# Kernel tuning notes

Measured on AMD Instinct MI355X. Metric: run time of the kernel, lower is better.

The kernel has to match this reference:

```python
import math
import jax, jax.numpy as jnp
import numpy as np

INPUT_DIM = 512
HIDDEN_DIM = 512
BATCH = 8
SEQ_LEN = 4096


def _xavier(key, shape):
    fan_out, fan_in = shape
    limit = math.sqrt(6.0 / (fan_in + fan_out))
    return jax.random.uniform(key, shape, jnp.float32, -limit, limit)


def setup_inputs() -> dict:
    key = jax.random.key(0)
    kx, kA, kB, kC, kD, kWg = jax.random.split(key, 6)
    return {
        "x": jax.random.normal(kx, (BATCH, SEQ_LEN, INPUT_DIM), jnp.float32),
        "A": jax.random.uniform(kA, (HIDDEN_DIM,), jnp.float32, 0.8, 0.95),
        "B": _xavier(kB, (HIDDEN_DIM, INPUT_DIM)),
        "C": _xavier(kC, (HIDDEN_DIM, HIDDEN_DIM)),
        "D": _xavier(kD, (HIDDEN_DIM, INPUT_DIM)),
        "Wg": _xavier(kWg, (HIDDEN_DIM, INPUT_DIM)),
        "bias_h": jnp.zeros((HIDDEN_DIM,), jnp.float32),
        "bias_y": jnp.zeros((HIDDEN_DIM,), jnp.float32),
    }


def reference(x, A, B, C, D, Wg, bias_h, bias_y):
    # x: (b, t, i). Eval mode: dropout is identity.
    hidden_dim = A.shape[0]
    # Precompute all input-dependent per-step terms as batched GEMMs.
    g = jnp.clip(jax.nn.sigmoid(jnp.einsum('bti,hi->bth', x, Wg)), 0.05, 0.95)
    xB = jnp.einsum('bti,hi->bth', x, B)
    # h_t = h_{t-1} + g_t*(A*h_{t-1} + xB_t + bias_h - h_{t-1})
    #     = (1 - g_t*(1 - A)) * h_{t-1} + g_t*(xB_t + bias_h)
    a_coef = 1.0 - g * (1.0 - A)          # (b, t, h)
    b_coef = g * (xB + bias_h)            # (b, t, h)

    def step(h, ab):
        a_t, b_t = ab
        h = a_t * h + b_t
        return h, h

    h0 = jnp.zeros((x.shape[0], hidden_dim), x.dtype)
    _, hs = jax.lax.scan(step, h0, (jnp.swapaxes(a_coef, 0, 1), jnp.swapaxes(b_coef, 0, 1)))
    hs = jnp.swapaxes(hs, 0, 1)           # (b, t, h)

    scale = 1.0 / math.sqrt(hidden_dim)
    y = (jnp.einsum('bth,oh->bto', hs, C) + jnp.einsum('bti,hi->bth', x, D) + bias_y) * scale
    return y
```

## Files before the change

kernel.cpp:

```cpp
#include <hip/hip_runtime.h>
#include <math.h>

#define MTOT 32768
#define KD 512
#define HD 512
#define NB 8
#define TS 4096
#define NCHUNK 64
#define TCHUNK 64

typedef __attribute__((ext_vector_type(8))) short bf16x8;
typedef __attribute__((ext_vector_type(4))) float f32x4;
typedef __attribute__((ext_vector_type(4))) unsigned short us4;

#define GLD16(gsrc, ldst) __builtin_amdgcn_global_load_lds( \
    (const __attribute__((address_space(1))) void*)(gsrc),   \
    (__attribute__((address_space(3))) void*)(ldst), 16, 0, 0)

__device__ __forceinline__ unsigned short f2bf(float f) {
    unsigned u = __float_as_uint(f);
    return (unsigned short)((u + 0x7FFFu + ((u >> 16) & 1u)) >> 16);
}
__device__ __forceinline__ float bf2f(unsigned short u) {
    return __uint_as_float(((unsigned)u) << 16);
}

__global__ __launch_bounds__(256) void cast_all(
    const float* __restrict__ x, const float* __restrict__ B,
    const float* __restrict__ G, const float* __restrict__ C,
    const float* __restrict__ D,
    unsigned short* __restrict__ x16, unsigned short* __restrict__ w16)
{
    const int blk = blockIdx.x;
    const float* src;
    unsigned short* dst;
    int i;
    if (blk < (MTOT * KD / 1024)) {
        src = x; dst = x16;
        i = blk * 1024 + threadIdx.x * 4;
    } else {
        const int r = blk - (MTOT * KD / 1024);
        const int mat = r >> 8;
        src = (mat == 0) ? B : (mat == 1) ? G : (mat == 2) ? C : D;
        dst = w16 + (size_t)mat * (HD * KD);
        i = (r & 255) * 1024 + threadIdx.x * 4;
    }
    float4 v = *(const float4*)(src + i);
    us4 o; o.x = f2bf(v.x); o.y = f2bf(v.y); o.z = f2bf(v.z); o.w = f2bf(v.w);
    *(us4*)(dst + i) = o;
}

__global__ __launch_bounds__(256, 2) void in_gemm_mfma(
    const short* __restrict__ xb, const short* __restrict__ wmat,
    const float* __restrict__ Avec, const float* __restrict__ bias_h,
    unsigned* __restrict__ ab16, float2* __restrict__ chPS)
{
    __shared__ __align__(16) short Xs[2][128 * 64];
    __shared__ __align__(16) short Ws[2][2][64 * 64];
    const int tid = threadIdx.x;
    const int w = tid >> 6, l = tid & 63;
    const int bid = blockIdx.x;
    const int xcd = bid & 7;
    const int jj  = bid >> 3;
    const int n0  = (jj & 7) * 64;
    const int m0  = (xcd * 32 + (jj >> 3)) * 128;
    const int wm = (w & 1) * 64;
    const int wn = (w >> 1) * 32;

    int xsrc[4], xdst[4];
    #pragma unroll
    for (int j = 0; j < 4; ++j) {
        const int s = (w * 4 + j) * 64 + l;
        const int r = s >> 3, g = (s & 7) ^ (r & 7);
        xsrc[j] = (m0 + r) * KD + g * 8;
        xdst[j] = (w * 4 + j) * 64 * 8;
    }
    int wsrc[2], wdst[2];
    #pragma unroll
    for (int j = 0; j < 2; ++j) {
        const int s = (w * 2 + j) * 64 + l;
        const int r = s >> 3, g = (s & 7) ^ (r & 7);
        wsrc[j] = (n0 + r) * KD + g * 8;
        wdst[j] = (w * 2 + j) * 64 * 8;
    }

#define STAGE_IN(TI, BUF) do {                                              \
    const int kk_ = (TI) * 64;                                              \
    _Pragma("unroll")                                                       \
    for (int j_ = 0; j_ < 4; ++j_)                                          \
        GLD16(xb + xsrc[j_] + kk_, &Xs[BUF][xdst[j_]]);                     \
    _Pragma("unroll")                                                       \
    for (int m_ = 0; m_ < 2; ++m_)                                          \
        _Pragma("unroll")                                                   \
        for (int j_ = 0; j_ < 2; ++j_)                                      \
            GLD16(wmat + (size_t)m_ * (HD * KD) + wsrc[j_] + kk_,           \
                  &Ws[BUF][m_][wdst[j_]]);                                  \
} while (0)

    f32x4 acc[2][4][2];
    #pragma unroll
    for (int a = 0; a < 2; ++a)
        #pragma unroll
        for (int i = 0; i < 4; ++i)
            #pragma unroll
            for (int j = 0; j < 2; ++j) acc[a][i][j] = (f32x4)0.0f;

    STAGE_IN(0, 0);
    STAGE_IN(1, 1);

    #pragma unroll
    for (int it = 0; it < 8; ++it) {
        const int cur = it & 1;
        if (it < 7) asm volatile("s_waitcnt vmcnt(8)" ::: "memory");
        else        asm volatile("s_waitcnt vmcnt(0)" ::: "memory");
        __builtin_amdgcn_s_barrier();
        __builtin_amdgcn_s_setprio(1);
        #pragma unroll
        for (int kc = 0; kc < 2; ++kc) {
            const int g = kc * 4 + (l >> 4);
            bf16x8 af[4];
            #pragma unroll
            for (int mt = 0; mt < 4; ++mt) {
                const int r = wm + mt * 16 + (l & 15);
                af[mt] = *(const bf16x8*)(&Xs[cur][r * 64 + ((g ^ (r & 7)) * 8)]);
            }
            #pragma unroll
            for (int mat = 0; mat < 2; ++mat) {
                #pragma unroll
                for (int nt = 0; nt < 2; ++nt) {
                    const int r = wn + nt * 16 + (l & 15);
                    bf16x8 bfv = *(const bf16x8*)(&Ws[cur][mat][r * 64 + ((g ^ (r & 7)) * 8)]);
                    #pragma unroll
                    for (int mt = 0; mt < 4; ++mt)
                        acc[mat][mt][nt] = __builtin_amdgcn_mfma_f32_16x16x32_bf16(
                            af[mt], bfv, acc[mat][mt][nt], 0, 0, 0);
                }
            }
        }
        __builtin_amdgcn_s_setprio(0);
        asm volatile("s_waitcnt lgkmcnt(0)" ::: "memory");
        __builtin_amdgcn_s_barrier();
        if (it < 6) STAGE_IN(it + 2, cur);
    }
#undef STAGE_IN

    const int q  = l >> 4;
    const int cl = l & 15;
    const int bidx   = m0 >> 12;
    const int c_in_b = ((m0 & (TS - 1)) >> 6) + (w & 1);
    #pragma unroll
    for (int nt = 0; nt < 2; ++nt) {
        const int n = n0 + wn + nt * 16 + cl;
        const float An1 = 1.0f - Avec[n];
        const float bh  = bias_h[n];
        float Pc = 1.0f, Sc = 0.0f;
        #pragma unroll
        for (int mt = 0; mt < 4; ++mt) {
            float Pl = 1.0f, Sl = 0.0f;
            #pragma unroll
            for (int r = 0; r < 4; ++r) {
                const float vB = acc[0][mt][nt][r];
                const float vG = acc[1][mt][nt][r];
                float g = __builtin_amdgcn_rcpf(1.0f + __expf(-vG));
                g = fminf(fmaxf(g, 0.05f), 0.95f);
                const unsigned short su = f2bf(g * An1);
                const unsigned short bu = f2bf(g * (vB + bh));
                const float a  = 1.0f - bf2f(su);
                const float bb = bf2f(bu);
                const int m = m0 + wm + mt * 16 + q * 4 + r;
                ab16[(size_t)m * HD + n] = (unsigned)su | ((unsigned)bu << 16);
                Sl = fmaf(a, Sl, bb);
                Pl *= a;
            }
            float Pm = 1.0f, Sm = 0.0f;
            #pragma unroll
            for (int k = 0; k < 4; ++k) {
                const float Pk = __shfl(Pl, cl + 16 * k, 64);
                const float Sk = __shfl(Sl, cl + 16 * k, 64);
                Sm = fmaf(Pk, Sm, Sk);
                Pm *= Pk;
            }
            Sc = fmaf(Pm, Sc, Sm);
            Pc *= Pm;
        }
        if (q == 0) {
            chPS[(size_t)c_in_b * (NB * HD) + bidx * HD + n] = make_float2(Pc, Sc);
        }
    }
}

__global__ __launch_bounds__(256) void scan_pass3(
    const unsigned* __restrict__ ab, const float2* __restrict__ chPS,
    unsigned short* __restrict__ hs_out)
{
    const int g = blockIdx.x * blockDim.x + threadIdx.x;
    const int h4 = (g & 127) * 4;
    const int rest = g >> 7;
    const int b = rest & (NB - 1);
    const int c = rest >> 3;
    const float2* p = chPS + (size_t)b * HD + h4;
    float hv0 = 0.0f, hv1 = 0.0f, hv2 = 0.0f, hv3 = 0.0f;
    for (int jc = 0; jc < c; ++jc) {
        const float4 ps01 = *(const float4*)(p + (size_t)jc * (NB * HD));
        const float4 ps23 = *(const float4*)(p + (size_t)jc * (NB * HD) + 2);
        hv0 = fmaf(ps01.x, hv0, ps01.y);
        hv1 = fmaf(ps01.z, hv1, ps01.w);
        hv2 = fmaf(ps23.x, hv2, ps23.y);
        hv3 = fmaf(ps23.z, hv3, ps23.w);
    }
    size_t idx = ((size_t)(b * TS + c * TCHUNK)) * HD + h4;
    #pragma unroll 4
    for (int t = 0; t < TCHUNK; ++t) {
        const uint4 v = *(const uint4*)(ab + idx);
        const float a0 = 1.0f - bf2f((unsigned short)(v.x & 0xFFFFu));
        const float a1 = 1.0f - bf2f((unsigned short)(v.y & 0xFFFFu));
        const float a2 = 1.0f - bf2f((unsigned short)(v.z & 0xFFFFu));
        const float a3 = 1.0f - bf2f((unsigned short)(v.w & 0xFFFFu));
        hv0 = fmaf(a0, hv0, bf2f((unsigned short)(v.x >> 16)));
        hv1 = fmaf(a1, hv1, bf2f((unsigned short)(v.y >> 16)));
        hv2 = fmaf(a2, hv2, bf2f((unsigned short)(v.z >> 16)));
        hv3 = fmaf(a3, hv3, bf2f((unsigned short)(v.w >> 16)));
        us4 o; o.x = f2bf(hv0); o.y = f2bf(hv1); o.z = f2bf(hv2); o.w = f2bf(hv3);
        *(us4*)(hs_out + idx) = o;
        idx += HD;
    }
}

__global__ __launch_bounds__(256, 2) void out_gemm_dual(
    const short* __restrict__ hs, const short* __restrict__ xb,
    const short* __restrict__ Cb, const short* __restrict__ Db,
    const float* __restrict__ bias_y, float* __restrict__ y)
{
    __shared__ __align__(16) short As[2][128 * 64];
    __shared__ __align__(16) short Ws[2][128 * 64];
    const int tid = threadIdx.x;
    const int w = tid >> 6, l = tid & 63;
    const int bid = blockIdx.x;
    const int xcd = bid & 7;
    const int jj  = bid >> 3;
    const int n0  = (jj & 3) * 128;
    const int m0  = (xcd * 32 + (jj >> 2)) * 128;
    const int wm = (w & 1) * 64;
    const int wn = (w >> 1) * 64;

    int aoff[4], woff[4], dst_s[4];
    #pragma unroll
    for (int j = 0; j < 4; ++j) {
        const int s = (w * 4 + j) * 64 + l;
        const int r = s >> 3, g = (s & 7) ^ (r & 7);
        aoff[j] = (m0 + r) * HD + g * 8;
        woff[j] = (n0 + r) * HD + g * 8;
        dst_s[j] = (w * 4 + j) * 64 * 8;
    }

#define STAGE_OUT(TI, BUF) do {                                         \
    const short* abase_ = (((TI) < 8) ? hs : xb) + ((TI) & 7) * 64;     \
    const short* wbase_ = (((TI) < 8) ? Cb : Db) + ((TI) & 7) * 64;     \
    _Pragma("unroll")                                                   \
    for (int j_ = 0; j_ < 4; ++j_) {                                    \
        GLD16(abase_ + aoff[j_], &As[BUF][dst_s[j_]]);                  \
        GLD16(wbase_ + woff[j_], &Ws[BUF][dst_s[j_]]);                  \
    }                                                                   \
} while (0)

    f32x4 acc[4][4];
    #pragma unroll
    for (int i = 0; i < 4; ++i)
        #pragma unroll
        for (int j = 0; j < 4; ++j) acc[i][j] = (f32x4)0.0f;

    STAGE_OUT(0, 0);
    STAGE_OUT(1, 1);

    #pragma unroll
    for (int ti = 0; ti < 16; ++ti) {
        const int cur = ti & 1;
        if (ti < 15) asm volatile("s_waitcnt vmcnt(8)" ::: "memory");
        else         asm volatile("s_waitcnt vmcnt(0)" ::: "memory");
        __builtin_amdgcn_s_barrier();
        __builtin_amdgcn_s_setprio(1);
        #pragma unroll
        for (int kc = 0; kc < 2; ++kc) {
            const int g = kc * 4 + (l >> 4);
            bf16x8 af[4], bfv[4];
            #pragma unroll
            for (int t = 0; t < 4; ++t) {
                const int ra = wm + t * 16 + (l & 15);
                af[t] = *(const bf16x8*)(&As[cur][ra * 64 + ((g ^ (ra & 7)) * 8)]);
                const int rb = wn + t * 16 + (l & 15);
                bfv[t] = *(const bf16x8*)(&Ws[cur][rb * 64 + ((g ^ (rb & 7)) * 8)]);
            }
            #pragma unroll
            for (int mt = 0; mt < 4; ++mt)
                #pragma unroll
                for (int nt = 0; nt < 4; ++nt)
                    acc[mt][nt] = __builtin_amdgcn_mfma_f32_16x16x32_bf16(
                        af[mt], bfv[nt], acc[mt][nt], 0, 0, 0);
        }
        __builtin_amdgcn_s_setprio(0);
        asm volatile("s_waitcnt lgkmcnt(0)" ::: "memory");
        __builtin_amdgcn_s_barrier();
        if (ti < 14) STAGE_OUT(ti + 2, cur);
    }
#undef STAGE_OUT

    const float scale = 0.04419417382415922f;
    #pragma unroll
    for (int nt = 0; nt < 4; ++nt) {
        const int n = n0 + wn + nt * 16 + (l & 15);
        const float by = bias_y[n];
        #pragma unroll
        for (int mt = 0; mt < 4; ++mt) {
            #pragma unroll
            for (int r = 0; r < 4; ++r) {
                const int m = m0 + wm + mt * 16 + (l >> 4) * 4 + r;
                y[(size_t)m * HD + n] = (acc[mt][nt][r] + by) * scale;
            }
        }
    }
}

extern "C" void kernel_launch(void* const* d_in, const int* in_sizes, int n_in,
                              void* d_out, int out_size, void* d_ws, size_t ws_size,
                              hipStream_t stream) {
    const float* x      = (const float*)d_in[0];
    const float* Avec   = (const float*)d_in[1];
    const float* Bw     = (const float*)d_in[2];
    const float* Cw     = (const float*)d_in[3];
    const float* Dw     = (const float*)d_in[4];
    const float* Wg     = (const float*)d_in[5];
    const float* bias_h = (const float*)d_in[6];
    const float* bias_y = (const float*)d_in[7];
    float* y = (float*)d_out;

    unsigned* ab16        = (unsigned*)d_ws;
    unsigned short* x16   = (unsigned short*)(ab16 + (size_t)MTOT * HD);
    unsigned short* hs16  = x16 + (size_t)MTOT * HD;
    unsigned short* w16   = hs16 + (size_t)MTOT * HD;
    float2* chPS = (float2*)(w16 + (size_t)4 * HD * KD);

    cast_all<<<MTOT * KD / 1024 + 4 * (HD * KD / 1024), 256, 0, stream>>>(
        x, Bw, Wg, Cw, Dw, x16, w16);

    in_gemm_mfma<<<2048, 256, 0, stream>>>(
        (const short*)x16, (const short*)w16, Avec, bias_h, ab16, chPS);

    scan_pass3<<<(NB * HD * NCHUNK / 4) / 256, 256, 0, stream>>>(ab16, chPS, hs16);

    out_gemm_dual<<<1024, 256, 0, stream>>>(
        (const short*)hs16, (const short*)x16,
        (const short*)(w16 + (size_t)2 * HD * KD),
        (const short*)(w16 + (size_t)3 * HD * KD), bias_y, y);
}
```

Baseline: 249.7 us.

## Load GEMM weight fragments directly into registers, bypassing LDS, and raise occupancy

In both the input and output GEMM kernels, weight tiles are no longer staged through LDS. Each wave instead reads its B-operand fragments straight from global memory into registers. Only the activation tile stays double-buffered in LDS, with the barrier and waitcnt sequence rearranged to match. The freed LDS allows the launch bounds to rise to 4 and 3 blocks per CU, aiming to improve latency hiding and remove LDS read traffic for weights. The risk is that the next iteration's MFMAs wait on global-load latency for the weights, which are issued only just before that iteration. Weight reads are also duplicated per wave instead of shared through LDS.

```diff
diff --git a/kernel.cpp b/kernel.cpp
--- a/kernel.cpp
+++ b/kernel.cpp
@@ -50,13 +50,12 @@
     *(us4*)(dst + i) = o;
 }
 
-__global__ __launch_bounds__(256, 2) void in_gemm_mfma(
+__global__ __launch_bounds__(256, 4) void in_gemm_mfma(
     const short* __restrict__ xb, const short* __restrict__ wmat,
     const float* __restrict__ Avec, const float* __restrict__ bias_h,
     unsigned* __restrict__ ab16, float2* __restrict__ chPS)
 {
     __shared__ __align__(16) short Xs[2][128 * 64];
-    __shared__ __align__(16) short Ws[2][2][64 * 64];
     const int tid = threadIdx.x;
     const int w = tid >> 6, l = tid & 63;
     const int bid = blockIdx.x;
@@ -75,26 +74,35 @@
         xsrc[j] = (m0 + r) * KD + g * 8;
         xdst[j] = (w * 4 + j) * 64 * 8;
     }
-    int wsrc[2], wdst[2];
-    #pragma unroll
-    for (int j = 0; j < 2; ++j) {
-        const int s = (w * 2 + j) * 64 + l;
-        const int r = s >> 3, g = (s & 7) ^ (r & 7);
-        wsrc[j] = (n0 + r) * KD + g * 8;
-        wdst[j] = (w * 2 + j) * 64 * 8;
-    }
-
-#define STAGE_IN(TI, BUF) do {                                              \
+
+    const int kg8 = (l >> 4) * 8;
+    size_t wofs[2][2];
+    #pragma unroll
+    for (int mat = 0; mat < 2; ++mat)
+        #pragma unroll
+        for (int nt = 0; nt < 2; ++nt)
+            wofs[mat][nt] = (size_t)mat * (HD * KD)
+                          + (size_t)(n0 + wn + nt * 16 + (l & 15)) * KD + kg8;
+
+    bf16x8 wf[2][2][2];
+
+#define STAGE_X(TI, BUF) do {                                               \
     const int kk_ = (TI) * 64;                                              \
     _Pragma("unroll")                                                       \
     for (int j_ = 0; j_ < 4; ++j_)                                          \
         GLD16(xb + xsrc[j_] + kk_, &Xs[BUF][xdst[j_]]);                     \
+} while (0)
+
+#define LOADW(TI) do {                                                      \
+    const int kk_ = (TI) * 64;                                              \
     _Pragma("unroll")                                                       \
-    for (int m_ = 0; m_ < 2; ++m_)                                          \
+    for (int mat_ = 0; mat_ < 2; ++mat_)                                    \
         _Pragma("unroll")                                                   \
-        for (int j_ = 0; j_ < 2; ++j_)                                      \
-            GLD16(wmat + (size_t)m_ * (HD * KD) + wsrc[j_] + kk_,           \
-                  &Ws[BUF][m_][wdst[j_]]);                                  \
+        for (int nt_ = 0; nt_ < 2; ++nt_)                                   \
+            _Pragma("unroll")                                               \
+            for (int kc_ = 0; kc_ < 2; ++kc_)                               \
+                wf[mat_][nt_][kc_] = *(const bf16x8*)(                      \
+                    wmat + wofs[mat_][nt_] + kk_ + kc_ * 32);               \
 } while (0)
 
     f32x4 acc[2][4][2];
@@ -105,15 +113,15 @@
             #pragma unroll
             for (int j = 0; j < 2; ++j) acc[a][i][j] = (f32x4)0.0f;
 
-    STAGE_IN(0, 0);
-    STAGE_IN(1, 1);
+    STAGE_X(0, 0);
+    LOADW(0);
+    STAGE_X(1, 1);
+    asm volatile("s_waitcnt vmcnt(4)" ::: "memory");
+    __builtin_amdgcn_s_barrier();
 
     #pragma unroll
     for (int it = 0; it < 8; ++it) {
         const int cur = it & 1;
-        if (it < 7) asm volatile("s_waitcnt vmcnt(8)" ::: "memory");
-        else        asm volatile("s_waitcnt vmcnt(0)" ::: "memory");
-        __builtin_amdgcn_s_barrier();
         __builtin_amdgcn_s_setprio(1);
         #pragma unroll
         for (int kc = 0; kc < 2; ++kc) {
@@ -125,24 +133,27 @@
                 af[mt] = *(const bf16x8*)(&Xs[cur][r * 64 + ((g ^ (r & 7)) * 8)]);
             }
             #pragma unroll
-            for (int mat = 0; mat < 2; ++mat) {
+            for (int mat = 0; mat < 2; ++mat)
                 #pragma unroll
-                for (int nt = 0; nt < 2; ++nt) {
-                    const int r = wn + nt * 16 + (l & 15);
-                    bf16x8 bfv = *(const bf16x8*)(&Ws[cur][mat][r * 64 + ((g ^ (r & 7)) * 8)]);
+                for (int nt = 0; nt < 2; ++nt)
                     #pragma unroll
                     for (int mt = 0; mt < 4; ++mt)
                         acc[mat][mt][nt] = __builtin_amdgcn_mfma_f32_16x16x32_bf16(
-                            af[mt], bfv, acc[mat][mt][nt], 0, 0, 0);
-                }
-            }
+                            af[mt], wf[mat][nt][kc], acc[mat][mt][nt], 0, 0, 0);
         }
         __builtin_amdgcn_s_setprio(0);
-        asm volatile("s_waitcnt lgkmcnt(0)" ::: "memory");
-        __builtin_amdgcn_s_barrier();
-        if (it < 6) STAGE_IN(it + 2, cur);
-    }
-#undef STAGE_IN
+        if (it < 7) {
+            LOADW(it + 1);
+            asm volatile("s_waitcnt lgkmcnt(0)" ::: "memory");
+            __builtin_amdgcn_s_barrier();
+            if (it < 6) STAGE_X(it + 2, cur);
+            if (it < 6) asm volatile("s_waitcnt vmcnt(12)" ::: "memory");
+            else        asm volatile("s_waitcnt vmcnt(8)" ::: "memory");
+            __builtin_amdgcn_s_barrier();
+        }
+    }
+#undef STAGE_X
+#undef LOADW
 
     const int q  = l >> 4;
     const int cl = l & 15;
@@ -226,13 +237,12 @@
     }
 }
 
-__global__ __launch_bounds__(256, 2) void out_gemm_dual(
+__global__ __launch_bounds__(256, 3) void out_gemm_dual(
     const short* __restrict__ hs, const short* __restrict__ xb,
     const short* __restrict__ Cb, const short* __restrict__ Db,
     const float* __restrict__ bias_y, float* __restrict__ y)
 {
     __shared__ __align__(16) short As[2][128 * 64];
-    __shared__ __align__(16) short Ws[2][128 * 64];
     const int tid = threadIdx.x;
     const int w = tid >> 6, l = tid & 63;
     const int bid = blockIdx.x;
@@ -243,66 +253,85 @@
     const int wm = (w & 1) * 64;
     const int wn = (w >> 1) * 64;
 
-    int aoff[4], woff[4], dst_s[4];
+    int aoff[4], dst_s[4];
     #pragma unroll
     for (int j = 0; j < 4; ++j) {
         const int s = (w * 4 + j) * 64 + l;
         const int r = s >> 3, g = (s & 7) ^ (r & 7);
         aoff[j] = (m0 + r) * HD + g * 8;
-        woff[j] = (n0 + r) * HD + g * 8;
         dst_s[j] = (w * 4 + j) * 64 * 8;
     }
 
-#define STAGE_OUT(TI, BUF) do {                                         \
+    const int kg8 = (l >> 4) * 8;
+    size_t wofs[4];
+    #pragma unroll
+    for (int nt = 0; nt < 4; ++nt)
+        wofs[nt] = (size_t)(n0 + wn + nt * 16 + (l & 15)) * HD + kg8;
+
+    bf16x8 wfo[4][2];
+
+#define STAGE_A(TI, BUF) do {                                           \
     const short* abase_ = (((TI) < 8) ? hs : xb) + ((TI) & 7) * 64;     \
-    const short* wbase_ = (((TI) < 8) ? Cb : Db) + ((TI) & 7) * 64;     \
     _Pragma("unroll")                                                   \
-    for (int j_ = 0; j_ < 4; ++j_) {                                    \
+    for (int j_ = 0; j_ < 4; ++j_)                                      \
         GLD16(abase_ + aoff[j_], &As[BUF][dst_s[j_]]);                  \
-        GLD16(wbase_ + woff[j_], &Ws[BUF][dst_s[j_]]);                  \
-    }                                                                   \
 } while (0)
 
+#define LOADW_OUT(TI) do {                                              \
+    const short* wb_ = (((TI) < 8) ? Cb : Db);                          \
+    const int kko_ = ((TI) & 7) * 64;                                   \
+    _Pragma("unroll")                                                   \
+    for (int nt_ = 0; nt_ < 4; ++nt_)                                   \
+        _Pragma("unroll")                                               \
+        for (int kc_ = 0; kc_ < 2; ++kc_)                               \
+            wfo[nt_][kc_] = *(const bf16x8*)(wb_ + wofs[nt_] + kko_ + kc_ * 32); \
+} while (0)
+
     f32x4 acc[4][4];
     #pragma unroll
     for (int i = 0; i < 4; ++i)
         #pragma unroll
         for (int j = 0; j < 4; ++j) acc[i][j] = (f32x4)0.0f;
 
-    STAGE_OUT(0, 0);
-    STAGE_OUT(1, 1);
+    STAGE_A(0, 0);
+    LOADW_OUT(0);
+    STAGE_A(1, 1);
+    asm volatile("s_waitcnt vmcnt(4)" ::: "memory");
+    __builtin_amdgcn_s_barrier();
 
     #pragma unroll
     for (int ti = 0; ti < 16; ++ti) {
         const int cur = ti & 1;
-        if (ti < 15) asm volatile("s_waitcnt vmcnt(8)" ::: "memory");
-        else         asm volatile("s_waitcnt vmcnt(0)" ::: "memory");
-        __builtin_amdgcn_s_barrier();
         __builtin_amdgcn_s_setprio(1);
         #pragma unroll
         for (int kc = 0; kc < 2; ++kc) {
             const int g = kc * 4 + (l >> 4);
-            bf16x8 af[4], bfv[4];
+            bf16x8 af[4];
             #pragma unroll
             for (int t = 0; t < 4; ++t) {
                 const int ra = wm + t * 16 + (l & 15);
                 af[t] = *(const bf16x8*)(&As[cur][ra * 64 + ((g ^ (ra & 7)) * 8)]);
-                const int rb = wn + t * 16 + (l & 15);
-                bfv[t] = *(const bf16x8*)(&Ws[cur][rb * 64 + ((g ^ (rb & 7)) * 8)]);
             }
             #pragma unroll
             for (int mt = 0; mt < 4; ++mt)
                 #pragma unroll
                 for (int nt = 0; nt < 4; ++nt)
                     acc[mt][nt] = __builtin_amdgcn_mfma_f32_16x16x32_bf16(
-                        af[mt], bfv[nt], acc[mt][nt], 0, 0, 0);
+                        af[mt], wfo[nt][kc], acc[mt][nt], 0, 0, 0);
         }
         __builtin_amdgcn_s_setprio(0);
-        asm volatile("s_waitcnt lgkmcnt(0)" ::: "memory");
-        __builtin_amdgcn_s_barrier();
-        if (ti < 14) STAGE_OUT(ti + 2, cur);
-    }
-#undef STAGE_OUT
+        if (ti < 15) {
+            LOADW_OUT(ti + 1);
+            asm volatile("s_waitcnt lgkmcnt(0)" ::: "memory");
+            __builtin_amdgcn_s_barrier();
+            if (ti < 14) STAGE_A(ti + 2, cur);
+            if (ti < 14) asm volatile("s_waitcnt vmcnt(12)" ::: "memory");
+            else         asm volatile("s_waitcnt vmcnt(8)" ::: "memory");
+            __builtin_amdgcn_s_barrier();
+        }
+    }
+#undef STAGE_A
+#undef LOADW_OUT
 
     const float scale = 0.04419417382415922f;
     #pragma unroll
```

Measured after the change: 313.8 us. +25.7%, slower.

## Replace double-buffered K pipeline with single-buffer dual-operand tiles in output GEMM

Applied to the files above, without the earlier changes.

The output GEMM no longer walks a 16-step K loop alternating between the hs/C and x/D halves with two ping-pong LDS buffers and manual vmcnt waits. Each of the 8 K steps now loads hs, x, C and D tiles together into four single buffers between two __syncthreads, then runs both MFMA sets. This halves the number of barrier rounds and the loop trip count, but drops the prefetch overlap, so global-load latency is exposed on every step. It also loses the setprio hints.

```diff
diff --git a/kernel.cpp b/kernel.cpp
--- a/kernel.cpp
+++ b/kernel.cpp
@@ -231,8 +231,10 @@
     const short* __restrict__ Cb, const short* __restrict__ Db,
     const float* __restrict__ bias_y, float* __restrict__ y)
 {
-    __shared__ __align__(16) short As[2][128 * 64];
-    __shared__ __align__(16) short Ws[2][128 * 64];
+    __shared__ __align__(16) short Hs[128 * 64];
+    __shared__ __align__(16) short Xs2[128 * 64];
+    __shared__ __align__(16) short Cs[128 * 64];
+    __shared__ __align__(16) short Ds[128 * 64];
     const int tid = threadIdx.x;
     const int w = tid >> 6, l = tid & 63;
     const int bid = blockIdx.x;
@@ -243,66 +245,69 @@
     const int wm = (w & 1) * 64;
     const int wn = (w >> 1) * 64;
 
-    int aoff[4], woff[4], dst_s[4];
+    int src_m[4], src_n[4], dst_s[4];
     #pragma unroll
     for (int j = 0; j < 4; ++j) {
         const int s = (w * 4 + j) * 64 + l;
         const int r = s >> 3, g = (s & 7) ^ (r & 7);
-        aoff[j] = (m0 + r) * HD + g * 8;
-        woff[j] = (n0 + r) * HD + g * 8;
+        src_m[j] = (m0 + r) * HD + g * 8;
+        src_n[j] = (n0 + r) * HD + g * 8;
         dst_s[j] = (w * 4 + j) * 64 * 8;
     }
 
-#define STAGE_OUT(TI, BUF) do {                                         \
-    const short* abase_ = (((TI) < 8) ? hs : xb) + ((TI) & 7) * 64;     \
-    const short* wbase_ = (((TI) < 8) ? Cb : Db) + ((TI) & 7) * 64;     \
-    _Pragma("unroll")                                                   \
-    for (int j_ = 0; j_ < 4; ++j_) {                                    \
-        GLD16(abase_ + aoff[j_], &As[BUF][dst_s[j_]]);                  \
-        GLD16(wbase_ + woff[j_], &Ws[BUF][dst_s[j_]]);                  \
-    }                                                                   \
-} while (0)
-
     f32x4 acc[4][4];
     #pragma unroll
     for (int i = 0; i < 4; ++i)
         #pragma unroll
         for (int j = 0; j < 4; ++j) acc[i][j] = (f32x4)0.0f;
 
-    STAGE_OUT(0, 0);
-    STAGE_OUT(1, 1);
-
-    #pragma unroll
-    for (int ti = 0; ti < 16; ++ti) {
-        const int cur = ti & 1;
-        if (ti < 15) asm volatile("s_waitcnt vmcnt(8)" ::: "memory");
-        else         asm volatile("s_waitcnt vmcnt(0)" ::: "memory");
-        __builtin_amdgcn_s_barrier();
-        __builtin_amdgcn_s_setprio(1);
+    for (int kk = 0; kk < HD; kk += 64) {
+        __syncthreads();
+        #pragma unroll
+        for (int j = 0; j < 4; ++j) {
+            GLD16(hs + src_m[j] + kk, Hs  + dst_s[j]);
+            GLD16(xb + src_m[j] + kk, Xs2 + dst_s[j]);
+            GLD16(Cb + src_n[j] + kk, Cs  + dst_s[j]);
+            GLD16(Db + src_n[j] + kk, Ds  + dst_s[j]);
+        }
+        __syncthreads();
         #pragma unroll
         for (int kc = 0; kc < 2; ++kc) {
             const int g = kc * 4 + (l >> 4);
-            bf16x8 af[4], bfv[4];
-            #pragma unroll
-            for (int t = 0; t < 4; ++t) {
-                const int ra = wm + t * 16 + (l & 15);
-                af[t] = *(const bf16x8*)(&As[cur][ra * 64 + ((g ^ (ra & 7)) * 8)]);
-                const int rb = wn + t * 16 + (l & 15);
-                bfv[t] = *(const bf16x8*)(&Ws[cur][rb * 64 + ((g ^ (rb & 7)) * 8)]);
-            }
-            #pragma unroll
-            for (int mt = 0; mt < 4; ++mt)
-                #pragma unroll
-                for (int nt = 0; nt < 4; ++nt)
-                    acc[mt][nt] = __builtin_amdgcn_mfma_f32_16x16x32_bf16(
-                        af[mt], bfv[nt], acc[mt][nt], 0, 0, 0);
-        }
-        __builtin_amdgcn_s_setprio(0);
-        asm volatile("s_waitcnt lgkmcnt(0)" ::: "memory");
-        __builtin_amdgcn_s_barrier();
-        if (ti < 14) STAGE_OUT(ti + 2, cur);
-    }
-#undef STAGE_OUT
+            {
+                bf16x8 af[4], bfv[4];
+                #pragma unroll
+                for (int t = 0; t < 4; ++t) {
+                    const int ra = wm + t * 16 + (l & 15);
+                    af[t] = *(const bf16x8*)(Hs + ra * 64 + ((g ^ (ra & 7)) * 8));
+                    const int rb = wn + t * 16 + (l & 15);
+                    bfv[t] = *(const bf16x8*)(Cs + rb * 64 + ((g ^ (rb & 7)) * 8));
+                }
+                #pragma unroll
+                for (int mt = 0; mt < 4; ++mt)
+                    #pragma unroll
+                    for (int nt = 0; nt < 4; ++nt)
+                        acc[mt][nt] = __builtin_amdgcn_mfma_f32_16x16x32_bf16(
+                            af[mt], bfv[nt], acc[mt][nt], 0, 0, 0);
+            }
+            {
+                bf16x8 af[4], bfv[4];
+                #pragma unroll
+                for (int t = 0; t < 4; ++t) {
+                    const int ra = wm + t * 16 + (l & 15);
+                    af[t] = *(const bf16x8*)(Xs2 + ra * 64 + ((g ^ (ra & 7)) * 8));
+                    const int rb = wn + t * 16 + (l & 15);
+                    bfv[t] = *(const bf16x8*)(Ds + rb * 64 + ((g ^ (rb & 7)) * 8));
+                }
+                #pragma unroll
+                for (int mt = 0; mt < 4; ++mt)
+                    #pragma unroll
+                    for (int nt = 0; nt < 4; ++nt)
+                        acc[mt][nt] = __builtin_amdgcn_mfma_f32_16x16x32_bf16(
+                            af[mt], bfv[nt], acc[mt][nt], 0, 0, 0);
+            }
+        }
+    }
 
     const float scale = 0.04419417382415922f;
     #pragma unroll
```

New measurement: 254.5 us. Within noise of the previous version (+1.9%).
